# Optimization experiments

Hardware: AMD Instinct MI355X
Metric: run time of the kernel (lower is better)

Reference implementation:

```python
import jax, jax.numpy as jnp
import numpy as np

N, NFEAT, NHID, NCLASS, NHEADS = 4096, 512, 64, 40, 8
ALPHA = 0.2
NEG = -9e15


def setup_inputs() -> dict:
    key = jax.random.key(0)
    ks = jax.random.split(key, 6)
    x = jax.random.normal(ks[0], (N, NFEAT), dtype=jnp.float32)
    adj = jax.random.randint(ks[1], (2, N, N), 0, 2, dtype=jnp.int32)
    # Xavier-ish scaled params
    W1 = jax.random.normal(ks[2], (NHEADS, NFEAT, NHID), dtype=jnp.float32) * (1.0 / np.sqrt(NFEAT))
    a1 = jax.random.normal(ks[3], (NHEADS, 2, NHID), dtype=jnp.float32) * (1.0 / np.sqrt(2 * NHID))
    Wo = jax.random.normal(ks[4], (NHEADS * NHID, NCLASS), dtype=jnp.float32) * (1.0 / np.sqrt(NHEADS * NHID))
    ao = jax.random.normal(ks[5], (2, NCLASS), dtype=jnp.float32) * (1.0 / np.sqrt(2 * NCLASS))
    return {"x": x, "adj": adj, "W1": W1, "a1": a1, "Wo": Wo, "ao": ao}


def _gat_layer(h, adj_mask, W, a_src, a_dst, concat):
    # h: [N,F]; W: [...,F,F']; a_src/a_dst: [...,F']
    if W.ndim == 3:  # multi-head: [H,F,F']
        Wh = jnp.einsum('nf,hfd->hnd', h, W)              # [H,N,F']
        f1 = jnp.einsum('hnd,hd->hn', Wh, a_src)           # [H,N]
        f2 = jnp.einsum('hnd,hd->hn', Wh, a_dst)
        e = jax.nn.leaky_relu(f1[:, :, None] + f2[:, None, :], ALPHA)  # [H,N,N]
        e = jnp.where(adj_mask[None], e, NEG)
        att = jax.nn.softmax(e, axis=-1)
        out = jnp.einsum('hnm,hmd->hnd', att, Wh)          # [H,N,F']
    else:
        Wh = h @ W                                         # [N,F']
        f1 = Wh @ a_src
        f2 = Wh @ a_dst
        e = jax.nn.leaky_relu(f1[:, None] + f2[None, :], ALPHA)
        e = jnp.where(adj_mask, e, NEG)
        att = jax.nn.softmax(e, axis=-1)
        out = att @ Wh
    return jax.nn.elu(out) if concat else out


def reference(x, adj, W1, a1, Wo, ao):
    adj1 = adj[1] > 0
    adj0 = adj[0] > 0
    # layer 1: NHEADS heads, concat=True
    h = _gat_layer(x, adj1, W1, a1[:, 0], a1[:, 1], concat=True)   # [H,N,NHID]
    h = jnp.transpose(h, (1, 0, 2)).reshape(x.shape[0], -1)        # [N, H*NHID]
    # output layer: concat=False, then outer ELU + log_softmax
    out = _gat_layer(h, adj0, Wo, ao[0], ao[1], concat=False)      # [N, NCLASS]
    out = jax.nn.elu(out)
    return jax.nn.log_softmax(out, axis=1)
```

## Files before the change

kernel.cpp:

```cpp
#include <hip/hip_runtime.h>
#include <hip/hip_bf16.h>

#define N      4096
#define NFEAT  512
#define NHID   64
#define NHEADS 8
#define NCLASS 40
#define ALPHA  0.2f
#define LOG2E  1.44269504f

typedef unsigned short u16;
typedef unsigned int   u32;
typedef __attribute__((ext_vector_type(8))) short bf16x8;
typedef __attribute__((ext_vector_type(4))) float f32x4;

__device__ __forceinline__ float b2f(u16 u) {
    return __uint_as_float(((u32)u) << 16);
}
__device__ __forceinline__ u32 rnd_hi(float f) {
    u32 u = __float_as_uint(f);
    return u + 0x7FFFu + ((u >> 16) & 1u);
}
__device__ __forceinline__ u32 pk2(float lo, float hi) {
    __hip_bfloat162 h = __float22bfloat162_rn(make_float2(lo, hi));
    return *(u32*)&h;
}
__device__ __forceinline__ u16 f2b(float f) {
    return (u16)(rnd_hi(f) >> 16);
}
__device__ __forceinline__ float mexp(int m, float t) {
    return m ? __builtin_amdgcn_exp2f(fmaxf(t, ALPHA * t)) : 0.f;
}
__device__ __forceinline__ bf16x8 ones_frag() {
    union { u16 u[8]; bf16x8 v; } o;
    #pragma unroll
    for (int j = 0; j < 8; ++j) o.u[j] = 0x3F80;
    return o.v;
}
__device__ __forceinline__ void gload_lds16(const u16* g, u16* l) {
    __builtin_amdgcn_global_load_lds(
        (const __attribute__((address_space(1))) void*)g,
        (__attribute__((address_space(3))) void*)l,
        16, 0, 0);
}

__global__ __launch_bounds__(256) void kcx(const float* __restrict__ x,
                                           u16* __restrict__ xb) {
    const int g = blockIdx.x * 256 + threadIdx.x;
    const size_t base = (size_t)g * 8;
    float4 v0 = *(const float4*)&x[base];
    float4 v1 = *(const float4*)&x[base + 4];
    uint4 o;
    o.x = pk2(v0.x, v0.y); o.y = pk2(v0.z, v0.w);
    o.z = pk2(v1.x, v1.y); o.w = pk2(v1.z, v1.w);
    *(uint4*)&xb[base] = o;
}

__global__ __launch_bounds__(256) void kcw(const float* __restrict__ W1,
                                           u16* __restrict__ W1b) {
    __shared__ float ts[64 * 68];
    const int t  = threadIdx.x;
    const int f0 = blockIdx.x * 64;
    const int h  = blockIdx.y;
    #pragma unroll
    for (int i = 0; i < 4; ++i) {
        int flat = t + 256 * i;
        int row = flat >> 4;
        int c4  = (flat & 15) * 4;
        *(float4*)&ts[row * 68 + c4] =
            *(const float4*)&W1[((size_t)h * 512 + f0 + row) * 64 + c4];
    }
    __syncthreads();
    const int d  = t >> 2;
    const int fs = (t & 3) * 16;
    u32 p[8];
    #pragma unroll
    for (int j = 0; j < 8; ++j)
        p[j] = pk2(ts[(fs + 2 * j) * 68 + d], ts[(fs + 2 * j + 1) * 68 + d]);
    u32* dst = (u32*)&W1b[((size_t)(h * 64 + d)) * 512 + f0 + fs];
    *(uint4*)dst       = make_uint4(p[0], p[1], p[2], p[3]);
    *(uint4*)(dst + 4) = make_uint4(p[4], p[5], p[6], p[7]);
}

__global__ __launch_bounds__(256, 4) void k1m_gemm1(const u16* __restrict__ xb,
                                                    const u16* __restrict__ W1b,
                                                    const float* __restrict__ a1,
                                                    u16* __restrict__ Wh1T,
                                                    float* __restrict__ F1,
                                                    float* __restrict__ F2) {
    __shared__ u16 xs[64 * 72];
    __shared__ u16 wvs[64 * 72];
    const int t    = threadIdx.x;
    const int n0   = blockIdx.x * 64;
    const int h    = blockIdx.y;
    const int lane = t & 63;
    const int l15  = lane & 15;
    const int q    = lane >> 4;
    const int wrow = (t >> 6) * 16;
    f32x4 acc[4];
    #pragma unroll
    for (int df = 0; df < 4; ++df)
        #pragma unroll
        for (int r = 0; r < 4; ++r) acc[df][r] = 0.f;
    for (int f0 = 0; f0 < 512; f0 += 64) {
        uint4 sx[2], sw[2];
        #pragma unroll
        for (int i = 0; i < 2; ++i) {
            int flat = t + 256 * i;
            int row = flat >> 3;
            int c8  = (flat & 7) * 8;
            sx[i] = *(const uint4*)&xb[(size_t)(n0 + row) * 512 + f0 + c8];
            sw[i] = *(const uint4*)&W1b[((size_t)(h * 64 + row)) * 512 + f0 + c8];
        }
        __syncthreads();
        #pragma unroll
        for (int i = 0; i < 2; ++i) {
            int flat = t + 256 * i;
            int row = flat >> 3;
            int c8  = (flat & 7) * 8;
            *(uint4*)&xs[row * 72 + c8]  = sx[i];
            *(uint4*)&wvs[row * 72 + c8] = sw[i];
        }
        __syncthreads();
        #pragma unroll
        for (int ks = 0; ks < 2; ++ks) {
            int k0 = ks * 32 + q * 8;
            bf16x8 a = *(const bf16x8*)&xs[(wrow + l15) * 72 + k0];
            #pragma unroll
            for (int df = 0; df < 4; ++df) {
                bf16x8 b = *(const bf16x8*)&wvs[(df * 16 + l15) * 72 + k0];
                acc[df] = __builtin_amdgcn_mfma_f32_16x16x32_bf16(a, b, acc[df], 0, 0, 0);
            }
        }
    }
    #pragma unroll
    for (int df = 0; df < 4; ++df) {
        uint2 o;
        o.x = pk2(acc[df][0], acc[df][1]);
        o.y = pk2(acc[df][2], acc[df][3]);
        *(uint2*)&Wh1T[((size_t)(h * 64 + df * 16 + l15)) * 4096 + n0 + wrow + q * 4] = o;
    }
    float a1v[4], a2v[4];
    #pragma unroll
    for (int df = 0; df < 4; ++df) {
        a1v[df] = a1[h * 128 + df * 16 + l15];
        a2v[df] = a1[h * 128 + 64 + df * 16 + l15];
    }
    #pragma unroll
    for (int r = 0; r < 4; ++r) {
        float s1 = 0.f, s2 = 0.f;
        #pragma unroll
        for (int df = 0; df < 4; ++df) {
            s1 += acc[df][r] * a1v[df];
            s2 += acc[df][r] * a2v[df];
        }
        #pragma unroll
        for (int off = 8; off >= 1; off >>= 1) {
            s1 += __shfl_xor(s1, off);
            s2 += __shfl_xor(s2, off);
        }
        if (l15 == 0) {
            int n = n0 + wrow + q * 4 + r;
            F1[h * 4096 + n] = s1 * LOG2E;
            F2[h * 4096 + n] = s2 * LOG2E;
        }
    }
}

__global__ __launch_bounds__(256, 4) void k3_attn1(const int* __restrict__ adj1,
                                                   const u16* __restrict__ Wh1T,
                                                   const float* __restrict__ F1,
                                                   const float* __restrict__ F2,
                                                   float* __restrict__ pacc1,
                                                   float* __restrict__ pz1) {
    __shared__ __align__(16) u16 wbf[64 * 136];
    __shared__ __align__(16) u16 whT[64 * 128];
    __shared__ float f1s[64];
    const int t     = threadIdx.x;
    const int n0    = blockIdx.x * 64;
    const int h     = blockIdx.y;
    const int chunk = blockIdx.z;
    const int lane  = t & 63;
    const int l15   = lane & 15;
    const int q     = lane >> 4;
    const int wrow  = (t >> 6) * 16;
    const int c4    = (t & 31) * 4;
    const int rg    = t >> 5;
    const bf16x8 bones = ones_frag();
    const int mbeg  = chunk * 2048;
    if (t < 64) f1s[t] = F1[h * N + n0 + t];

    const int wv   = t >> 6;
    const int lsub = lane >> 4;
    const int slot = lane & 15;
    const u16* gsrc[4];
    #pragma unroll
    for (int i = 0; i < 4; ++i) {
        int row_l = wv * 16 + i * 4 + lsub;
        int sc    = (slot ^ ((i * 4 + lsub) & 7)) * 8;
        gsrc[i] = Wh1T + ((size_t)(h * 64 + row_l)) * 4096 + sc;
    }
    u16* ldst = &whT[wv * 2048];
    const int xb7 = l15 & 7;

    f32x4 acc[5];
    #pragma unroll
    for (int df = 0; df < 5; ++df)
        #pragma unroll
        for (int r = 0; r < 4; ++r) acc[df][r] = 0.f;

    int4 aprev[8];
    #pragma unroll
    for (int i = 0; i < 8; ++i)
        aprev[i] = *(const int4*)&adj1[(size_t)(n0 + rg + 8 * i) * N + mbeg + c4];
    __syncthreads();

    for (int m0 = mbeg; m0 < mbeg + 2048; m0 += 128) {
        #pragma unroll
        for (int i = 0; i < 4; ++i)
            gload_lds16(gsrc[i] + m0, ldst + i * 512);
        float4 F2v = *(const float4*)&F2[h * N + m0 + c4];
        #pragma unroll
        for (int i = 0; i < 8; ++i) {
            int rr = rg + 8 * i;
            int4 a4 = aprev[i];
            float f1v = f1s[rr];
            float w0 = mexp(a4.x, f1v + F2v.x);
            float w1 = mexp(a4.y, f1v + F2v.y);
            float w2 = mexp(a4.z, f1v + F2v.z);
            float w3 = mexp(a4.w, f1v + F2v.w);
            uint2 pk;
            pk.x = pk2(w0, w1);
            pk.y = pk2(w2, w3);
            *(uint2*)&wbf[rr * 136 + c4] = pk;
        }
        int mn = (m0 + 128 < mbeg + 2048) ? m0 + 128 : mbeg;
        #pragma unroll
        for (int i = 0; i < 8; ++i)
            aprev[i] = *(const int4*)&adj1[(size_t)(n0 + rg + 8 * i) * N + mn + c4];
        __syncthreads();
        #pragma unroll
        for (int ks = 0; ks < 4; ++ks) {
            int k0 = ks * 32 + q * 8;
            bf16x8 a = *(const bf16x8*)&wbf[(wrow + l15) * 136 + k0];
            #pragma unroll
            for (int df = 0; df < 4; ++df) {
                bf16x8 b = *(const bf16x8*)
                    &whT[(df * 16 + l15) * 128 + (((ks * 4 + q) ^ xb7) * 8)];
                acc[df] = __builtin_amdgcn_mfma_f32_16x16x32_bf16(a, b, acc[df], 0, 0, 0);
            }
            acc[4] = __builtin_amdgcn_mfma_f32_16x16x32_bf16(a, bones, acc[4], 0, 0, 0);
        }
        __syncthreads();
    }
    const size_t rowbase = (size_t)(chunk * 8 + h) * 4096 + n0;
    #pragma unroll
    for (int r = 0; r < 4; ++r) {
        int nl = wrow + q * 4 + r;
        if (l15 == 0) pz1[rowbase + nl] = acc[4][r];
        #pragma unroll
        for (int df = 0; df < 4; ++df)
            pacc1[(rowbase + nl) * 64 + df * 16 + l15] = acc[df][r];
    }
}

__global__ __launch_bounds__(256) void k3b_norm(const float* __restrict__ pacc1,
                                                const float* __restrict__ pz1,
                                                float* __restrict__ h1) {
    const int g = blockIdx.x * 256 + threadIdx.x;
    const int d = g & 63;
    const int h = (g >> 6) & 7;
    const int n = g >> 9;
    const size_t i0 = (size_t)h * 4096 + n;
    float s = pacc1[i0 * 64 + d] + pacc1[(i0 + 8 * 4096) * 64 + d];
    float z = pz1[i0] + pz1[i0 + 8 * 4096];
    float v = s / fmaxf(z, 1e-30f);
    h1[(size_t)n * 512 + h * 64 + d] = v > 0.f ? v : __expf(v) - 1.f;
}

__global__ __launch_bounds__(256) void k4_gemm2(const float* __restrict__ h1,
                                                const float* __restrict__ Wo,
                                                const float* __restrict__ ao,
                                                float* __restrict__ F1o,
                                                float* __restrict__ F2o,
                                                u16* __restrict__ Wh2T) {
    const int t = threadIdx.x;
    const int c = t & 63;
    const int n = blockIdx.x * 4 + (t >> 6);
    float acc = 0.f;
    if (c < NCLASS) {
        const float* hrow = &h1[(size_t)n * 512];
        #pragma unroll 8
        for (int f = 0; f < 512; ++f)
            acc += hrow[f] * Wo[f * NCLASS + c];
        Wh2T[(size_t)c * 4096 + n] = f2b(acc);
    }
    float s1 = (c < NCLASS) ? acc * ao[c] : 0.f;
    float s2 = (c < NCLASS) ? acc * ao[NCLASS + c] : 0.f;
    #pragma unroll
    for (int off = 32; off >= 1; off >>= 1) {
        s1 += __shfl_xor(s1, off);
        s2 += __shfl_xor(s2, off);
    }
    if (c == 0) {
        F1o[n] = s1 * LOG2E;
        F2o[n] = s2 * LOG2E;
    }
}

__global__ __launch_bounds__(256, 5) void k5a_attn2(const int* __restrict__ adj0,
                                                    const u16* __restrict__ Wh2T,
                                                    const float* __restrict__ F1o,
                                                    const float* __restrict__ F2o,
                                                    float* __restrict__ pacc,
                                                    float* __restrict__ pz) {
    __shared__ __align__(16) u16 wbf[64 * 136];
    __shared__ __align__(16) u16 whT[48 * 128];
    __shared__ float f1s[64];
    const int t     = threadIdx.x;
    const int n0    = blockIdx.x * 64;
    const int chunk = blockIdx.y;
    const int mbase = chunk * 256;
    const int lane  = t & 63;
    const int l15   = lane & 15;
    const int q     = lane >> 4;
    const int wrow  = (t >> 6) * 16;
    const int c4    = (t & 31) * 4;
    const int rg    = t >> 5;
    const bf16x8 bones = ones_frag();
    if (t < 64) f1s[t] = F1o[n0 + t];
    #pragma unroll
    for (int i = 0; i < 4; ++i)
        whT[40 * 128 + t + 256 * i] = 0;

    const int wv   = t >> 6;
    const int lsub = lane >> 4;
    const int slot = lane & 15;
    const int ninst = (wv < 2) ? 4 : ((wv == 2) ? 2 : 0);
    const u16* gsrc[4];
    #pragma unroll
    for (int i = 0; i < 4; ++i) {
        int row_l = wv * 16 + i * 4 + lsub;
        int rl    = (row_l < 40) ? row_l : 0;
        int sc    = (slot ^ ((i * 4 + lsub) & 7)) * 8;
        gsrc[i] = Wh2T + (size_t)rl * 4096 + sc;
    }
    u16* ldst = &whT[wv * 2048];
    const int xb7 = l15 & 7;

    f32x4 acc[4];
    #pragma unroll
    for (int df = 0; df < 4; ++df)
        #pragma unroll
        for (int r = 0; r < 4; ++r) acc[df][r] = 0.f;

    int4 aprev[8];
    #pragma unroll
    for (int i = 0; i < 8; ++i)
        aprev[i] = *(const int4*)&adj0[(size_t)(n0 + rg + 8 * i) * N + mbase + c4];
    __syncthreads();

    #pragma unroll
    for (int mt = 0; mt < 2; ++mt) {
        const int m0 = mbase + mt * 128;
        #pragma unroll
        for (int i = 0; i < 4; ++i)
            if (i < ninst)
                gload_lds16(gsrc[i] + m0, ldst + i * 512);
        float4 F2v = *(const float4*)&F2o[m0 + c4];
        #pragma unroll
        for (int i = 0; i < 8; ++i) {
            int rr = rg + 8 * i;
            int4 a4 = aprev[i];
            float f1v = f1s[rr];
            float w0 = mexp(a4.x, f1v + F2v.x);
            float w1 = mexp(a4.y, f1v + F2v.y);
            float w2 = mexp(a4.z, f1v + F2v.z);
            float w3 = mexp(a4.w, f1v + F2v.w);
            uint2 pk;
            pk.x = pk2(w0, w1);
            pk.y = pk2(w2, w3);
            *(uint2*)&wbf[rr * 136 + c4] = pk;
        }
        int mn = mbase + ((mt + 1) & 1) * 128;
        #pragma unroll
        for (int i = 0; i < 8; ++i)
            aprev[i] = *(const int4*)&adj0[(size_t)(n0 + rg + 8 * i) * N + mn + c4];
        __syncthreads();
        #pragma unroll
        for (int ks = 0; ks < 4; ++ks) {
            int k0 = ks * 32 + q * 8;
            bf16x8 a = *(const bf16x8*)&wbf[(wrow + l15) * 136 + k0];
            #pragma unroll
            for (int df = 0; df < 3; ++df) {
                bf16x8 b = *(const bf16x8*)
                    &whT[(df * 16 + l15) * 128 + (((ks * 4 + q) ^ xb7) * 8)];
                acc[df] = __builtin_amdgcn_mfma_f32_16x16x32_bf16(a, b, acc[df], 0, 0, 0);
            }
            acc[3] = __builtin_amdgcn_mfma_f32_16x16x32_bf16(a, bones, acc[3], 0, 0, 0);
        }
        __syncthreads();
    }
    #pragma unroll
    for (int r = 0; r < 4; ++r) {
        int n = n0 + wrow + q * 4 + r;
        if (l15 == 0) pz[(size_t)chunk * N + n] = acc[3][r];
        #pragma unroll
        for (int df = 0; df < 3; ++df) {
            int c = df * 16 + l15;
            if (c < NCLASS)
                pacc[((size_t)chunk * N + n) * NCLASS + c] = acc[df][r];
        }
    }
}

__global__ __launch_bounds__(256) void k5b_final(const float* __restrict__ pacc,
                                                 const float* __restrict__ pz,
                                                 float* __restrict__ out) {
    const int t = threadIdx.x;
    const int lane = t & 63;
    const int n = blockIdx.x * 4 + (t >> 6);
    float s = 0.f, Z = 0.f;
    #pragma unroll
    for (int ch = 0; ch < 16; ++ch) {
        Z += pz[(size_t)ch * N + n];
        if (lane < NCLASS) s += pacc[(size_t)(ch * N + n) * NCLASS + lane];
    }
    float v;
    if (lane < NCLASS) {
        v = s / fmaxf(Z, 1e-30f);
        v = v > 0.f ? v : __expf(v) - 1.f;
    } else {
        v = -INFINITY;
    }
    float mx = v;
    #pragma unroll
    for (int off = 32; off >= 1; off >>= 1) mx = fmaxf(mx, __shfl_xor(mx, off));
    float ex = (lane < NCLASS) ? __expf(v - mx) : 0.f;
    #pragma unroll
    for (int off = 32; off >= 1; off >>= 1) ex += __shfl_xor(ex, off);
    float lse = mx + __logf(ex);
    if (lane < NCLASS) out[(size_t)n * NCLASS + lane] = v - lse;
}

extern "C" void kernel_launch(void* const* d_in, const int* in_sizes, int n_in,
                              void* d_out, int out_size, void* d_ws, size_t ws_size,
                              hipStream_t stream) {
    const float* x   = (const float*)d_in[0];
    const int*   adj = (const int*)d_in[1];
    const float* W1  = (const float*)d_in[2];
    const float* a1  = (const float*)d_in[3];
    const float* Wo  = (const float*)d_in[4];
    const float* ao  = (const float*)d_in[5];

    float* ws    = (float*)d_ws;
    float* h1    = ws;
    float* F1    = h1 + 2097152;
    float* F2    = F1 + 32768;
    float* F1o   = F2 + 32768;
    float* F2o   = F1o + 4096;
    float* pz    = F2o + 4096;
    float* pz1   = pz + 65536;
    u16*   Wh1T  = (u16*)(pz1 + 65536);
    u16*   Wh2T  = Wh1T + 2097152;
    float* R     = (float*)(Wh2T + 163840);
    u16*   xb    = (u16*)R;
    u16*   W1b   = xb + 2097152;
    float* pacc1 = R;
    float* pacc  = R;

    const int* adj0 = adj;
    const int* adj1 = adj + (size_t)N * N;

    hipLaunchKernelGGL(kcx,       dim3(1024),     dim3(256), 0, stream, x, xb);
    hipLaunchKernelGGL(kcw,       dim3(8, 8),     dim3(256), 0, stream, W1, W1b);
    hipLaunchKernelGGL(k1m_gemm1, dim3(64, 8),    dim3(256), 0, stream, xb, W1b, a1, Wh1T, F1, F2);
    hipLaunchKernelGGL(k3_attn1,  dim3(64, 8, 2), dim3(256), 0, stream, adj1, Wh1T, F1, F2, pacc1, pz1);
    hipLaunchKernelGGL(k3b_norm,  dim3(8192),     dim3(256), 0, stream, pacc1, pz1, h1);
    hipLaunchKernelGGL(k4_gemm2,  dim3(1024),     dim3(256), 0, stream, h1, Wo, ao, F1o, F2o, Wh2T);
    hipLaunchKernelGGL(k5a_attn2, dim3(64, 16),   dim3(256), 0, stream, adj0, Wh2T, F1o, F2o, pacc, pz);
    hipLaunchKernelGGL(k5b_final, dim3(1024),     dim3(256), 0, stream, pacc, pz, (float*)d_out);
}
```

Baseline: 323.0 us.

## Fuse layer-1 attention normalization into attn kernel, drop split-K over neighbors

The layer-1 attention kernel no longer splits the neighbor dimension into two chunks. Each block now walks all 4096 neighbors and applies the softmax normalization and ELU in its epilogue, writing h1 directly. This removes the k3b_norm launch and the partial-sum round trip through global memory. In exchange the grid shrinks from 1024 to 512 blocks and each block's serial loop doubles, which may reduce parallelism. Both attention kernels also interleave the next-tile adjacency loads with the exp computation and prefetch F2 one tile ahead, and k5a's occupancy hint drops from 5 to 4.

```diff
diff --git a/kernel.cpp b/kernel.cpp
--- a/kernel.cpp
+++ b/kernel.cpp
@@ -171,15 +171,13 @@
                                                    const u16* __restrict__ Wh1T,
                                                    const float* __restrict__ F1,
                                                    const float* __restrict__ F2,
-                                                   float* __restrict__ pacc1,
-                                                   float* __restrict__ pz1) {
+                                                   float* __restrict__ h1) {
     __shared__ __align__(16) u16 wbf[64 * 136];
     __shared__ __align__(16) u16 whT[64 * 128];
     __shared__ float f1s[64];
     const int t     = threadIdx.x;
     const int n0    = blockIdx.x * 64;
     const int h     = blockIdx.y;
-    const int chunk = blockIdx.z;
     const int lane  = t & 63;
     const int l15   = lane & 15;
     const int q     = lane >> 4;
@@ -187,7 +185,6 @@
     const int c4    = (t & 31) * 4;
     const int rg    = t >> 5;
     const bf16x8 bones = ones_frag();
-    const int mbeg  = chunk * 2048;
     if (t < 64) f1s[t] = F1[h * N + n0 + t];
 
     const int wv   = t >> 6;
@@ -212,18 +209,22 @@
     int4 aprev[8];
     #pragma unroll
     for (int i = 0; i < 8; ++i)
-        aprev[i] = *(const int4*)&adj1[(size_t)(n0 + rg + 8 * i) * N + mbeg + c4];
+        aprev[i] = *(const int4*)&adj1[(size_t)(n0 + rg + 8 * i) * N + c4];
+    float4 f2n = *(const float4*)&F2[h * N + c4];
     __syncthreads();
 
-    for (int m0 = mbeg; m0 < mbeg + 2048; m0 += 128) {
+    for (int m0 = 0; m0 < 4096; m0 += 128) {
         #pragma unroll
         for (int i = 0; i < 4; ++i)
             gload_lds16(gsrc[i] + m0, ldst + i * 512);
-        float4 F2v = *(const float4*)&F2[h * N + m0 + c4];
+        const float4 F2v = f2n;
+        const int mn = (m0 + 128 < 4096) ? m0 + 128 : 0;
+        f2n = *(const float4*)&F2[h * N + mn + c4];
         #pragma unroll
         for (int i = 0; i < 8; ++i) {
-            int rr = rg + 8 * i;
+            const int rr = rg + 8 * i;
             int4 a4 = aprev[i];
+            aprev[i] = *(const int4*)&adj1[(size_t)(n0 + rr) * N + mn + c4];
             float f1v = f1s[rr];
             float w0 = mexp(a4.x, f1v + F2v.x);
             float w1 = mexp(a4.y, f1v + F2v.y);
@@ -234,10 +235,6 @@
             pk.y = pk2(w2, w3);
             *(uint2*)&wbf[rr * 136 + c4] = pk;
         }
-        int mn = (m0 + 128 < mbeg + 2048) ? m0 + 128 : mbeg;
-        #pragma unroll
-        for (int i = 0; i < 8; ++i)
-            aprev[i] = *(const int4*)&adj1[(size_t)(n0 + rg + 8 * i) * N + mn + c4];
         __syncthreads();
         #pragma unroll
         for (int ks = 0; ks < 4; ++ks) {
@@ -253,29 +250,17 @@
         }
         __syncthreads();
     }
-    const size_t rowbase = (size_t)(chunk * 8 + h) * 4096 + n0;
     #pragma unroll
     for (int r = 0; r < 4; ++r) {
-        int nl = wrow + q * 4 + r;
-        if (l15 == 0) pz1[rowbase + nl] = acc[4][r];
-        #pragma unroll
-        for (int df = 0; df < 4; ++df)
-            pacc1[(rowbase + nl) * 64 + df * 16 + l15] = acc[df][r];
-    }
-}
-
-__global__ __launch_bounds__(256) void k3b_norm(const float* __restrict__ pacc1,
-                                                const float* __restrict__ pz1,
-                                                float* __restrict__ h1) {
-    const int g = blockIdx.x * 256 + threadIdx.x;
-    const int d = g & 63;
-    const int h = (g >> 6) & 7;
-    const int n = g >> 9;
-    const size_t i0 = (size_t)h * 4096 + n;
-    float s = pacc1[i0 * 64 + d] + pacc1[(i0 + 8 * 4096) * 64 + d];
-    float z = pz1[i0] + pz1[i0 + 8 * 4096];
-    float v = s / fmaxf(z, 1e-30f);
-    h1[(size_t)n * 512 + h * 64 + d] = v > 0.f ? v : __expf(v) - 1.f;
+        const int nl = wrow + q * 4 + r;
+        const float z = fmaxf(acc[4][r], 1e-30f);
+        #pragma unroll
+        for (int df = 0; df < 4; ++df) {
+            float v = acc[df][r] / z;
+            v = v > 0.f ? v : __expf(v) - 1.f;
+            h1[(size_t)(n0 + nl) * 512 + h * 64 + df * 16 + l15] = v;
+        }
+    }
 }
 
 __global__ __launch_bounds__(256) void k4_gemm2(const float* __restrict__ h1,
@@ -308,7 +293,7 @@
     }
 }
 
-__global__ __launch_bounds__(256, 5) void k5a_attn2(const int* __restrict__ adj0,
+__global__ __launch_bounds__(256, 4) void k5a_attn2(const int* __restrict__ adj0,
                                                     const u16* __restrict__ Wh2T,
                                                     const float* __restrict__ F1o,
                                                     const float* __restrict__ F2o,
@@ -358,6 +343,7 @@
     #pragma unroll
     for (int i = 0; i < 8; ++i)
         aprev[i] = *(const int4*)&adj0[(size_t)(n0 + rg + 8 * i) * N + mbase + c4];
+    float4 f2n = *(const float4*)&F2o[mbase + c4];
     __syncthreads();
 
     #pragma unroll
@@ -367,11 +353,14 @@
         for (int i = 0; i < 4; ++i)
             if (i < ninst)
                 gload_lds16(gsrc[i] + m0, ldst + i * 512);
-        float4 F2v = *(const float4*)&F2o[m0 + c4];
+        const float4 F2v = f2n;
+        const int mn = mbase + ((mt + 1) & 1) * 128;
+        f2n = *(const float4*)&F2o[mn + c4];
         #pragma unroll
         for (int i = 0; i < 8; ++i) {
-            int rr = rg + 8 * i;
+            const int rr = rg + 8 * i;
             int4 a4 = aprev[i];
+            aprev[i] = *(const int4*)&adj0[(size_t)(n0 + rr) * N + mn + c4];
             float f1v = f1s[rr];
             float w0 = mexp(a4.x, f1v + F2v.x);
             float w1 = mexp(a4.y, f1v + F2v.y);
@@ -382,10 +371,6 @@
             pk.y = pk2(w2, w3);
             *(uint2*)&wbf[rr * 136 + c4] = pk;
         }
-        int mn = mbase + ((mt + 1) & 1) * 128;
-        #pragma unroll
-        for (int i = 0; i < 8; ++i)
-            aprev[i] = *(const int4*)&adj0[(size_t)(n0 + rg + 8 * i) * N + mn + c4];
         __syncthreads();
         #pragma unroll
         for (int ks = 0; ks < 4; ++ks) {
@@ -466,18 +451,16 @@
     float* R     = (float*)(Wh2T + 163840);
     u16*   xb    = (u16*)R;
     u16*   W1b   = xb + 2097152;
-    float* pacc1 = R;
     float* pacc  = R;
 
     const int* adj0 = adj;
     const int* adj1 = adj + (size_t)N * N;
 
-    hipLaunchKernelGGL(kcx,       dim3(1024),     dim3(256), 0, stream, x, xb);
-    hipLaunchKernelGGL(kcw,       dim3(8, 8),     dim3(256), 0, stream, W1, W1b);
-    hipLaunchKernelGGL(k1m_gemm1, dim3(64, 8),    dim3(256), 0, stream, xb, W1b, a1, Wh1T, F1, F2);
-    hipLaunchKernelGGL(k3_attn1,  dim3(64, 8, 2), dim3(256), 0, stream, adj1, Wh1T, F1, F2, pacc1, pz1);
-    hipLaunchKernelGGL(k3b_norm,  dim3(8192),     dim3(256), 0, stream, pacc1, pz1, h1);
-    hipLaunchKernelGGL(k4_gemm2,  dim3(1024),     dim3(256), 0, stream, h1, Wo, ao, F1o, F2o, Wh2T);
-    hipLaunchKernelGGL(k5a_attn2, dim3(64, 16),   dim3(256), 0, stream, adj0, Wh2T, F1o, F2o, pacc, pz);
-    hipLaunchKernelGGL(k5b_final, dim3(1024),     dim3(256), 0, stream, pacc, pz, (float*)d_out);
-}
+    hipLaunchKernelGGL(kcx,       dim3(1024),   dim3(256), 0, stream, x, xb);
+    hipLaunchKernelGGL(kcw,       dim3(8, 8),   dim3(256), 0, stream, W1, W1b);
+    hipLaunchKernelGGL(k1m_gemm1, dim3(64, 8),  dim3(256), 0, stream, xb, W1b, a1, Wh1T, F1, F2);
+    hipLaunchKernelGGL(k3_attn1,  dim3(64, 8),  dim3(256), 0, stream, adj1, Wh1T, F1, F2, h1);
+    hipLaunchKernelGGL(k4_gemm2,  dim3(1024),   dim3(256), 0, stream, h1, Wo, ao, F1o, F2o, Wh2T);
+    hipLaunchKernelGGL(k5a_attn2, dim3(64, 16), dim3(256), 0, stream, adj0, Wh2T, F1o, F2o, pacc, pz);
+    hipLaunchKernelGGL(k5b_final, dim3(1024),   dim3(256), 0, stream, pacc, pz, (float*)d_out);
+}
```

New measurement: 331.6 us. +2.7%, slower.
